# Kernel optimization log

Measured on AMD Instinct MI355X. Metric: run time of the kernel, lower is better.

## Reference

```python
import jax, jax.numpy as jnp
import numpy as np

E = 131072      # edges per key
MUL = 64        # multiplicity in '64x0e+64x1o'
FEA = MUL * 4   # 64 scalars + 64*3 vector components = 256
RAD = 64        # edge-length embedding width (64x0e)
HID = 128       # MLP hidden (128x0e)
WNUM = 4 * MUL  # 4 uvu paths x 64 per-channel weights = 256


def _mlp(x, W1, b1, g, be, W2):
    # Linear -> LayerNorm -> Gate(silu on scalars) -> last Linear (no bias)
    h = x @ W1 + b1
    mu = h.mean(-1, keepdims=True)
    var = h.var(-1, keepdims=True)
    h = (h - mu) / jnp.sqrt(var + 1e-5) * g + be
    return jax.nn.silu(h) @ W2


def _dtp(fea, vec, w):
    # depthwise (uvu) tensor product of (64x0e+64x1o) x (1x0e+1x1o) -> (64x0e+64x1o)
    x0 = fea[:, :MUL]                       # [E, 64]   0e part
    x1 = fea[:, MUL:].reshape(-1, MUL, 3)   # [E, 64, 3] 1o part
    y0 = vec[:, 0]                          # [E]       0e
    y1 = vec[:, 1:4]                        # [E, 3]    1o
    w1, w2, w3, w4 = jnp.split(w, 4, axis=1)  # each [E, 64]
    inv_s3 = 1.0 / jnp.sqrt(jnp.asarray(3.0, fea.dtype))  # CG(1,1,0) = delta/sqrt(3)
    inv_s2 = 1.0 / jnp.sqrt(jnp.asarray(2.0, fea.dtype))  # per-output path normalization (2 paths each)
    out0 = (w1 * x0 * y0[:, None]
            + w4 * jnp.einsum('eud,ed->eu', x1, y1) * inv_s3) * inv_s2
    out1 = (w2[:, :, None] * x0[:, :, None] * y1[:, None, :]
            + w3[:, :, None] * x1 * y0[:, None, None]) * inv_s2
    return jnp.concatenate([out0, out1.reshape(-1, MUL * 3)], axis=1)


def setup_inputs() -> dict:
    key = jax.random.key(0)
    ks = jax.random.split(key, 16)
    d = {}
    for i, k in enumerate(['a', 'b']):
        d[f'edge_fea_{k}'] = jax.random.normal(ks[i * 3 + 0], (E, FEA), jnp.float32)
        d[f'edge_vec_{k}'] = jax.random.normal(ks[i * 3 + 1], (E, 4), jnp.float32)
        d[f'edge_len_{k}'] = jax.random.uniform(ks[i * 3 + 2], (E, RAD), jnp.float32)
        d[f'W1_{k}'] = jax.random.normal(ks[6 + i * 2], (RAD, HID), jnp.float32) / np.sqrt(RAD)
        d[f'b1_{k}'] = jnp.zeros((HID,), jnp.float32)
        d[f'g_{k}'] = jnp.ones((HID,), jnp.float32)
        d[f'be_{k}'] = jnp.zeros((HID,), jnp.float32)
        d[f'W2_{k}'] = jax.random.normal(ks[10 + i * 2], (HID, WNUM), jnp.float32) / np.sqrt(HID)
    return d


def reference(edge_fea_a, edge_vec_a, edge_len_a, W1_a, b1_a, g_a, be_a, W2_a,
              edge_fea_b, edge_vec_b, edge_len_b, W1_b, b1_b, g_b, be_b, W2_b):
    wa = _mlp(edge_len_a, W1_a, b1_a, g_a, be_a, W2_a)
    wb = _mlp(edge_len_b, W1_b, b1_b, g_b, be_b, W2_b)
    return (_dtp(edge_fea_a, edge_vec_a, wa), _dtp(edge_fea_b, edge_vec_b, wb))
```

## Files before the change

kernel.cpp:

```cpp
#include <hip/hip_runtime.h>

namespace {
constexpr int E_N  = 131072;
constexpr int FEA  = 256;
constexpr int RAD  = 64;
constexpr int HID  = 128;
constexpr int WN   = 256;
constexpr int EPB  = 64;
constexpr int NT   = 256;
constexpr int LSTR = 68;
constexpr int ASTR = 132;
constexpr int SMEMF = EPB * ASTR;
constexpr int FRAG_HI_SHORTS = 2 * 4 * 16 * 64 * 8;
constexpr int W1HI = 2 * FRAG_HI_SHORTS;
constexpr int W1LO_DELTA = 2 * 2 * 8 * 64 * 8;
}

typedef short short8v __attribute__((ext_vector_type(8)));
typedef float floatx4 __attribute__((ext_vector_type(4)));

__device__ __forceinline__ unsigned bf16rne(float x) {
    const unsigned u = __float_as_uint(x);
    return (u + 0x7FFFu + ((u >> 16) & 1u)) >> 16;
}
__device__ __forceinline__ float bf16tof(unsigned h) {
    return __uint_as_float(h << 16);
}
__device__ __forceinline__ void bf16split(float x, unsigned& hi, unsigned& lo) {
    hi = bf16rne(x);
    lo = bf16rne(x - bf16tof(hi));
}

union FragU { uint4 u; short8v v; };

__global__ __launch_bounds__(64)
void prep_w2(const float* __restrict__ W2a, const float* __restrict__ W2b,
             unsigned short* __restrict__ frag)
{
    const int lane = threadIdx.x;
    const int nb = blockIdx.x, kt = blockIdx.y, pipe = blockIdx.z;
    const float* __restrict__ W2 = pipe ? W2b : W2a;
    const int g = lane >> 4, s = lane & 15;
    unsigned ph[4], pl[4];
    #pragma unroll
    for (int p = 0; p < 4; ++p) {
        const float x0 = W2[(size_t)(32*kt + 8*g + 2*p)     * WN + nb*16 + s];
        const float x1 = W2[(size_t)(32*kt + 8*g + 2*p + 1) * WN + nb*16 + s];
        unsigned h0, l0, h1, l1;
        bf16split(x0, h0, l0);
        bf16split(x1, h1, l1);
        ph[p] = h0 | (h1 << 16);
        pl[p] = l0 | (l1 << 16);
    }
    const size_t fi = (size_t)pipe * 32768 + (size_t)((kt*16 + nb)*64 + lane) * 8;
    *(uint4*)(frag + fi)                  = make_uint4(ph[0], ph[1], ph[2], ph[3]);
    *(uint4*)(frag + FRAG_HI_SHORTS + fi) = make_uint4(pl[0], pl[1], pl[2], pl[3]);
}

__global__ __launch_bounds__(64)
void prep_w1(const float* __restrict__ W1a, const float* __restrict__ W1b,
             unsigned short* __restrict__ frag)
{
    const int lane = threadIdx.x;
    const int nb = blockIdx.x, kt = blockIdx.y, pipe = blockIdx.z;
    const float* __restrict__ W1 = pipe ? W1b : W1a;
    const int g = lane >> 4, s = lane & 15;
    unsigned ph[4], pl[4];
    #pragma unroll
    for (int p = 0; p < 4; ++p) {
        const float x0 = W1[(size_t)(32*kt + 8*g + 2*p)     * HID + nb*16 + s];
        const float x1 = W1[(size_t)(32*kt + 8*g + 2*p + 1) * HID + nb*16 + s];
        unsigned h0, l0, h1, l1;
        bf16split(x0, h0, l0);
        bf16split(x1, h1, l1);
        ph[p] = h0 | (h1 << 16);
        pl[p] = l0 | (l1 << 16);
    }
    const size_t fi = (size_t)W1HI + (size_t)pipe * 8192
                    + (size_t)((kt*8 + nb)*64 + lane) * 8;
    *(uint4*)(frag + fi)              = make_uint4(ph[0], ph[1], ph[2], ph[3]);
    *(uint4*)(frag + W1LO_DELTA + fi) = make_uint4(pl[0], pl[1], pl[2], pl[3]);
}

__global__ __launch_bounds__(NT, 4)
void fused_mlp_dtp(
    const float* __restrict__ fea_a, const float* __restrict__ vec_a,
    const float* __restrict__ len_a, const float* __restrict__ b1_a,
    const float* __restrict__ g_a,   const float* __restrict__ be_a,
    const float* __restrict__ fea_b, const float* __restrict__ vec_b,
    const float* __restrict__ len_b, const float* __restrict__ b1_b,
    const float* __restrict__ g_b,   const float* __restrict__ be_b,
    const unsigned short* __restrict__ fragW,
    float* __restrict__ out)
{
    __shared__ __align__(16) float smem[SMEMF];

    const int pipe = blockIdx.y;
    const float* __restrict__ fea = pipe ? fea_b : fea_a;
    const float* __restrict__ vec = pipe ? vec_b : vec_a;
    const float* __restrict__ len = pipe ? len_b : len_a;
    const float* __restrict__ b1  = pipe ? b1_b  : b1_a;
    const float* __restrict__ g   = pipe ? g_b   : g_a;
    const float* __restrict__ be  = pipe ? be_b  : be_a;
    float* __restrict__ outp = out + (size_t)pipe * (size_t)E_N * FEA;

    const int t    = threadIdx.x;
    const int lane = t & 63;
    const int wv_  = t >> 6;
    const int s_   = lane & 15, g_ = lane >> 4;
    const long e0  = (long)blockIdx.x * EPB;

    {
        const float4* __restrict__ src = (const float4*)(len + e0 * RAD);
        #pragma unroll
        for (int i = 0; i < (EPB * RAD / 4) / NT; ++i) {
            const int f = t + i * NT;
            const float4 v = src[f];
            const int e = f >> 4, kq = (f & 15) * 4;
            *(float4*)(&smem[e * LSTR + kq]) = v;
        }
    }
    __syncthreads();

    floatx4 acc2[8];
    #pragma unroll
    for (int nb = 0; nb < 8; ++nb) {
        acc2[nb][0] = 0.f; acc2[nb][1] = 0.f; acc2[nb][2] = 0.f; acc2[nb][3] = 0.f;
    }
    {
        const int eA = wv_ * 16 + s_;
        const unsigned short* __restrict__ fH1 = fragW + W1HI + (size_t)pipe * 8192;
        const unsigned short* __restrict__ fL1 = fH1 + W1LO_DELTA;
        #pragma unroll
        for (int kt = 0; kt < 2; ++kt) {
            float xs[8];
            {
                const float4 x0 = *(const float4*)(&smem[eA*LSTR + 32*kt + 8*g_]);
                const float4 x1 = *(const float4*)(&smem[eA*LSTR + 32*kt + 8*g_ + 4]);
                xs[0]=x0.x; xs[1]=x0.y; xs[2]=x0.z; xs[3]=x0.w;
                xs[4]=x1.x; xs[5]=x1.y; xs[6]=x1.z; xs[7]=x1.w;
            }
            FragU ahu, alu;
            {
                unsigned ph[4], pl[4];
                #pragma unroll
                for (int p = 0; p < 4; ++p) {
                    unsigned h0, l0, h1, l1;
                    bf16split(xs[2*p],     h0, l0);
                    bf16split(xs[2*p + 1], h1, l1);
                    ph[p] = h0 | (h1 << 16);
                    pl[p] = l0 | (l1 << 16);
                }
                ahu.u = make_uint4(ph[0], ph[1], ph[2], ph[3]);
                alu.u = make_uint4(pl[0], pl[1], pl[2], pl[3]);
            }
            const short8v ah = ahu.v, al = alu.v;
            const size_t kb = (size_t)(kt * 8) * 512 + (size_t)lane * 8;
            #pragma unroll
            for (int nb = 0; nb < 8; ++nb) {
                const short8v bh = *(const short8v*)(fH1 + kb + nb * 512);
                const short8v bl = *(const short8v*)(fL1 + kb + nb * 512);
                acc2[nb] = __builtin_amdgcn_mfma_f32_16x16x32_bf16(ah, bh, acc2[nb], 0, 0, 0);
                acc2[nb] = __builtin_amdgcn_mfma_f32_16x16x32_bf16(ah, bl, acc2[nb], 0, 0, 0);
                acc2[nb] = __builtin_amdgcn_mfma_f32_16x16x32_bf16(al, bh, acc2[nb], 0, 0, 0);
            }
        }
    }
    __syncthreads();

    {
        float hv[8][4];
        float sum[4] = {0.f, 0.f, 0.f, 0.f};
        float sq [4] = {0.f, 0.f, 0.f, 0.f};
        #pragma unroll
        for (int nb = 0; nb < 8; ++nb) {
            const float b1v = b1[16*nb + s_];
            #pragma unroll
            for (int r = 0; r < 4; ++r) {
                const float v = acc2[nb][r] + b1v;
                hv[nb][r] = v;
                sum[r] += v;
                sq [r] += v * v;
            }
        }
        float mu[4], iv[4];
        #pragma unroll
        for (int r = 0; r < 4; ++r) {
            float s1 = sum[r], s2 = sq[r];
            s1 += __shfl_xor(s1, 1); s1 += __shfl_xor(s1, 2);
            s1 += __shfl_xor(s1, 4); s1 += __shfl_xor(s1, 8);
            s2 += __shfl_xor(s2, 1); s2 += __shfl_xor(s2, 2);
            s2 += __shfl_xor(s2, 4); s2 += __shfl_xor(s2, 8);
            mu[r] = s1 * (1.0f / HID);
            float var = s2 * (1.0f / HID) - mu[r] * mu[r];
            var = fmaxf(var, 0.0f);
            iv[r] = rsqrtf(var + 1e-5f);
        }
        const int rowb = wv_ * 16 + 4 * g_;
        #pragma unroll
        for (int nb = 0; nb < 8; ++nb) {
            const float gv  = g [16*nb + s_];
            const float bev = be[16*nb + s_];
            #pragma unroll
            for (int r = 0; r < 4; ++r) {
                const float hn = (hv[nb][r] - mu[r]) * iv[r] * gv + bev;
                const float sl = hn / (1.0f + __expf(-hn));
                smem[(rowb + r) * ASTR + 16*nb + s_] = sl;
            }
        }
    }
    __syncthreads();

    floatx4 acc[16];
    #pragma unroll
    for (int nb = 0; nb < 16; ++nb) {
        acc[nb][0] = 0.f; acc[nb][1] = 0.f; acc[nb][2] = 0.f; acc[nb][3] = 0.f;
    }
    {
        const int eA = wv_ * 16 + s_;
        const unsigned short* __restrict__ fH = fragW + (size_t)pipe * 32768;
        const unsigned short* __restrict__ fL = fH + FRAG_HI_SHORTS;
        for (int kt = 0; kt < 4; ++kt) {
            float xs[8];
            {
                const float4 x0 = *(const float4*)(&smem[eA*ASTR + 32*kt + 8*g_]);
                const float4 x1 = *(const float4*)(&smem[eA*ASTR + 32*kt + 8*g_ + 4]);
                xs[0]=x0.x; xs[1]=x0.y; xs[2]=x0.z; xs[3]=x0.w;
                xs[4]=x1.x; xs[5]=x1.y; xs[6]=x1.z; xs[7]=x1.w;
            }
            FragU ahu, alu;
            {
                unsigned ph[4], pl[4];
                #pragma unroll
                for (int p = 0; p < 4; ++p) {
                    unsigned h0, l0, h1, l1;
                    bf16split(xs[2*p],     h0, l0);
                    bf16split(xs[2*p + 1], h1, l1);
                    ph[p] = h0 | (h1 << 16);
                    pl[p] = l0 | (l1 << 16);
                }
                ahu.u = make_uint4(ph[0], ph[1], ph[2], ph[3]);
                alu.u = make_uint4(pl[0], pl[1], pl[2], pl[3]);
            }
            const short8v ah = ahu.v, al = alu.v;
            const size_t kb = (size_t)(kt * 16) * 512 + (size_t)lane * 8;
            #pragma unroll
            for (int nb = 0; nb < 16; ++nb) {
                const short8v bh = *(const short8v*)(fH + kb + nb * 512);
                const short8v bl = *(const short8v*)(fL + kb + nb * 512);
                acc[nb] = __builtin_amdgcn_mfma_f32_16x16x32_bf16(ah, bh, acc[nb], 0, 0, 0);
                acc[nb] = __builtin_amdgcn_mfma_f32_16x16x32_bf16(ah, bl, acc[nb], 0, 0, 0);
                acc[nb] = __builtin_amdgcn_mfma_f32_16x16x32_bf16(al, bh, acc[nb], 0, 0, 0);
            }
        }
    }
    __syncthreads();

    {
        const float c2 = 0.70710678118654752f;
        const float c3 = 0.40824829046386302f;
        float* sStage = smem + wv_ * 784;
        for (int r = 0; r < 4; ++r) {
            const long e = e0 + wv_ * 16 + 4 * g_ + r;
            const float4 y = *(const float4*)(vec + e * 4);
            const float* __restrict__ fr   = fea  + e * (size_t)FEA;
            float* __restrict__       orow = outp + e * (size_t)FEA;
            #pragma unroll
            for (int q = 0; q < 4; ++q) {
                const int u = 16 * q + s_;
                const float w1 = acc[q     ][r];
                const float w2 = acc[q + 4 ][r];
                const float w3 = acc[q + 8 ][r];
                const float w4 = acc[q + 12][r];
                const float x0  = fr[u];
                const float x1a = fr[64 + 3*u + 0];
                const float x1b = fr[64 + 3*u + 1];
                const float x1c = fr[64 + 3*u + 2];
                const float dot = x1a*y.y + x1b*y.z + x1c*y.w;
                orow[u] = w1*x0*y.x*c2 + w4*dot*c3;
                sStage[g_*196 + 3*u + 0] = (w2*x0*y.y + w3*x1a*y.x) * c2;
                sStage[g_*196 + 3*u + 1] = (w2*x0*y.z + w3*x1b*y.x) * c2;
                sStage[g_*196 + 3*u + 2] = (w2*x0*y.w + w3*x1c*y.x) * c2;
            }
            __syncthreads();
            #pragma unroll
            for (int rr = 0; rr < 3; ++rr) {
                const int flat = rr * 256 + lane * 4;
                const int eloc = flat / 192;
                const int pos  = flat % 192;
                const float4 v = *(const float4*)(&sStage[eloc * 196 + pos]);
                *(float4*)(&outp[(e0 + wv_*16 + 4*eloc + r) * (size_t)FEA + 64 + pos]) = v;
            }
            __syncthreads();
        }
    }
}

extern "C" void kernel_launch(void* const* d_in, const int* in_sizes, int n_in,
                              void* d_out, int out_size, void* d_ws, size_t ws_size,
                              hipStream_t stream) {
    (void)in_sizes; (void)n_in; (void)ws_size; (void)out_size;
    const float* fea_a = (const float*)d_in[0];
    const float* vec_a = (const float*)d_in[1];
    const float* len_a = (const float*)d_in[2];
    const float* W1_a  = (const float*)d_in[3];
    const float* b1_a  = (const float*)d_in[4];
    const float* g_a   = (const float*)d_in[5];
    const float* be_a  = (const float*)d_in[6];
    const float* W2_a  = (const float*)d_in[7];
    const float* fea_b = (const float*)d_in[8];
    const float* vec_b = (const float*)d_in[9];
    const float* len_b = (const float*)d_in[10];
    const float* W1_b  = (const float*)d_in[11];
    const float* b1_b  = (const float*)d_in[12];
    const float* g_b   = (const float*)d_in[13];
    const float* be_b  = (const float*)d_in[14];
    const float* W2_b  = (const float*)d_in[15];
    float* out = (float*)d_out;
    unsigned short* frag = (unsigned short*)d_ws;

    hipLaunchKernelGGL(prep_w2, dim3(16, 4, 2), dim3(64), 0, stream,
                       W2_a, W2_b, frag);
    hipLaunchKernelGGL(prep_w1, dim3(8, 2, 2), dim3(64), 0, stream,
                       W1_a, W1_b, frag);

    dim3 grid(E_N / EPB, 2);
    dim3 block(NT);
    hipLaunchKernelGGL(fused_mlp_dtp, grid, block, 0, stream,
                       fea_a, vec_a, len_a, b1_a, g_a, be_a,
                       fea_b, vec_b, len_b, b1_b, g_b, be_b,
                       frag, out);
}
```

Measured before the change: 180.9 us.

## Store activations as pre-split bf16 in swizzled LDS and drop block barriers

The LayerNorm/SiLU stage now writes hi/lo bf16 halves of each activation into XOR-swizzled LDS, so the second GEMM loads ready-made MFMA fragments instead of re-splitting floats per kt. Block-wide __syncthreads are replaced with wave-local lgkmcnt waits, on the basis that each wave reads only rows it wrote itself. LDS is reorganized to 32KB and launch bounds are raised to 5 blocks per SM to improve occupancy. The risk is the wave-local fence: the final staging region (wave*4096 bytes) overlaps activation rows that other waves may still be reading, which could race.

```diff
diff --git a/kernel.cpp b/kernel.cpp
--- a/kernel.cpp
+++ b/kernel.cpp
@@ -9,8 +9,6 @@
 constexpr int EPB  = 64;
 constexpr int NT   = 256;
 constexpr int LSTR = 68;
-constexpr int ASTR = 132;
-constexpr int SMEMF = EPB * ASTR;
 constexpr int FRAG_HI_SHORTS = 2 * 4 * 16 * 64 * 8;
 constexpr int W1HI = 2 * FRAG_HI_SHORTS;
 constexpr int W1LO_DELTA = 2 * 2 * 8 * 64 * 8;
@@ -30,6 +28,11 @@
     hi = bf16rne(x);
     lo = bf16rne(x - bf16tof(hi));
 }
+
+#define LDS_FENCE() do { \
+    asm volatile("s_waitcnt lgkmcnt(0)" ::: "memory"); \
+    __builtin_amdgcn_sched_barrier(0); \
+} while (0)
 
 union FragU { uint4 u; short8v v; };
 
@@ -82,7 +85,7 @@
     *(uint4*)(frag + W1LO_DELTA + fi) = make_uint4(pl[0], pl[1], pl[2], pl[3]);
 }
 
-__global__ __launch_bounds__(NT, 4)
+__global__ __launch_bounds__(NT, 5)
 void fused_mlp_dtp(
     const float* __restrict__ fea_a, const float* __restrict__ vec_a,
     const float* __restrict__ len_a, const float* __restrict__ b1_a,
@@ -93,7 +96,10 @@
     const unsigned short* __restrict__ fragW,
     float* __restrict__ out)
 {
-    __shared__ __align__(16) float smem[SMEMF];
+    __shared__ __align__(16) char smemraw[32768];
+    float*          lenT = (float*)smemraw;
+    unsigned short* actH = (unsigned short*)smemraw;
+    unsigned short* actL = (unsigned short*)(smemraw + 16384);
 
     const int pipe = blockIdx.y;
     const float* __restrict__ fea = pipe ? fea_b : fea_a;
@@ -117,7 +123,7 @@
             const int f = t + i * NT;
             const float4 v = src[f];
             const int e = f >> 4, kq = (f & 15) * 4;
-            *(float4*)(&smem[e * LSTR + kq]) = v;
+            *(float4*)(&lenT[e * LSTR + kq]) = v;
         }
     }
     __syncthreads();
@@ -135,8 +141,8 @@
         for (int kt = 0; kt < 2; ++kt) {
             float xs[8];
             {
-                const float4 x0 = *(const float4*)(&smem[eA*LSTR + 32*kt + 8*g_]);
-                const float4 x1 = *(const float4*)(&smem[eA*LSTR + 32*kt + 8*g_ + 4]);
+                const float4 x0 = *(const float4*)(&lenT[eA*LSTR + 32*kt + 8*g_]);
+                const float4 x1 = *(const float4*)(&lenT[eA*LSTR + 32*kt + 8*g_ + 4]);
                 xs[0]=x0.x; xs[1]=x0.y; xs[2]=x0.z; xs[3]=x0.w;
                 xs[4]=x1.x; xs[5]=x1.y; xs[6]=x1.z; xs[7]=x1.w;
             }
@@ -201,15 +207,21 @@
         for (int nb = 0; nb < 8; ++nb) {
             const float gv  = g [16*nb + s_];
             const float bev = be[16*nb + s_];
+            const int blkbase = 2*nb + (s_ >> 3);
             #pragma unroll
             for (int r = 0; r < 4; ++r) {
                 const float hn = (hv[nb][r] - mu[r]) * iv[r] * gv + bev;
                 const float sl = hn / (1.0f + __expf(-hn));
-                smem[(rowb + r) * ASTR + 16*nb + s_] = sl;
-            }
-        }
-    }
-    __syncthreads();
+                unsigned h, l;
+                bf16split(sl, h, l);
+                const int e = rowb + r;
+                const int idx = e * 128 + ((blkbase ^ (e & 7)) << 3) + (s_ & 7);
+                actH[idx] = (unsigned short)h;
+                actL[idx] = (unsigned short)l;
+            }
+        }
+    }
+    LDS_FENCE();
 
     floatx4 acc[16];
     #pragma unroll
@@ -221,27 +233,10 @@
         const unsigned short* __restrict__ fH = fragW + (size_t)pipe * 32768;
         const unsigned short* __restrict__ fL = fH + FRAG_HI_SHORTS;
         for (int kt = 0; kt < 4; ++kt) {
-            float xs[8];
-            {
-                const float4 x0 = *(const float4*)(&smem[eA*ASTR + 32*kt + 8*g_]);
-                const float4 x1 = *(const float4*)(&smem[eA*ASTR + 32*kt + 8*g_ + 4]);
-                xs[0]=x0.x; xs[1]=x0.y; xs[2]=x0.z; xs[3]=x0.w;
-                xs[4]=x1.x; xs[5]=x1.y; xs[6]=x1.z; xs[7]=x1.w;
-            }
+            const int sg = (4*kt + g_) ^ (s_ & 7);
             FragU ahu, alu;
-            {
-                unsigned ph[4], pl[4];
-                #pragma unroll
-                for (int p = 0; p < 4; ++p) {
-                    unsigned h0, l0, h1, l1;
-                    bf16split(xs[2*p],     h0, l0);
-                    bf16split(xs[2*p + 1], h1, l1);
-                    ph[p] = h0 | (h1 << 16);
-                    pl[p] = l0 | (l1 << 16);
-                }
-                ahu.u = make_uint4(ph[0], ph[1], ph[2], ph[3]);
-                alu.u = make_uint4(pl[0], pl[1], pl[2], pl[3]);
-            }
+            ahu.u = *(const uint4*)(actH + eA * 128 + sg * 8);
+            alu.u = *(const uint4*)(actL + eA * 128 + sg * 8);
             const short8v ah = ahu.v, al = alu.v;
             const size_t kb = (size_t)(kt * 16) * 512 + (size_t)lane * 8;
             #pragma unroll
@@ -254,12 +249,12 @@
             }
         }
     }
-    __syncthreads();
+    LDS_FENCE();
 
     {
         const float c2 = 0.70710678118654752f;
         const float c3 = 0.40824829046386302f;
-        float* sStage = smem + wv_ * 784;
+        float* sStage = (float*)(smemraw + wv_ * 4096);
         for (int r = 0; r < 4; ++r) {
             const long e = e0 + wv_ * 16 + 4 * g_ + r;
             const float4 y = *(const float4*)(vec + e * 4);
@@ -282,7 +277,7 @@
                 sStage[g_*196 + 3*u + 1] = (w2*x0*y.z + w3*x1b*y.x) * c2;
                 sStage[g_*196 + 3*u + 2] = (w2*x0*y.w + w3*x1c*y.x) * c2;
             }
-            __syncthreads();
+            LDS_FENCE();
             #pragma unroll
             for (int rr = 0; rr < 3; ++rr) {
                 const int flat = rr * 256 + lane * 4;
@@ -291,7 +286,7 @@
                 const float4 v = *(const float4*)(&sStage[eloc * 196 + pos]);
                 *(float4*)(&outp[(e0 + wv_*16 + 4*eloc + r) * (size_t)FEA + 64 + pos]) = v;
             }
-            __syncthreads();
+            LDS_FENCE();
         }
     }
 }
```

Result: slower. 298.2 us (+64.8%).

## Process two 16-row M-blocks per wave to reuse weight fragments

Applied to the files above, without the earlier changes.

Doubles edges per block from 64 to 128 so each wave computes two 16-edge MFMA row tiles, reusing every loaded W1/W2 bf16 fragment across both tiles. This halves weight-fragment global/L2 loads per edge and the number of blocks. In exchange accumulator register use roughly doubles, so launch bounds drop to 2 blocks per SM-equivalent, lowering occupancy for the memory-bound DTP epilogue. The shared-memory buffer is sized from EPB, so its size grows with the tile.

```diff
diff --git a/kernel.cpp b/kernel.cpp
--- a/kernel.cpp
+++ b/kernel.cpp
@@ -6,7 +6,7 @@
 constexpr int RAD  = 64;
 constexpr int HID  = 128;
 constexpr int WN   = 256;
-constexpr int EPB  = 64;
+constexpr int EPB  = 128;
 constexpr int NT   = 256;
 constexpr int LSTR = 68;
 constexpr int ASTR = 132;
@@ -82,7 +82,7 @@
     *(uint4*)(frag + W1LO_DELTA + fi) = make_uint4(pl[0], pl[1], pl[2], pl[3]);
 }
 
-__global__ __launch_bounds__(NT, 4)
+__global__ __launch_bounds__(NT, 2)
 void fused_mlp_dtp(
     const float* __restrict__ fea_a, const float* __restrict__ vec_a,
     const float* __restrict__ len_a, const float* __restrict__ b1_a,
@@ -108,6 +108,7 @@
     const int lane = t & 63;
     const int wv_  = t >> 6;
     const int s_   = lane & 15, g_ = lane >> 4;
+    const int ew   = wv_ * 32;
     const long e0  = (long)blockIdx.x * EPB;
 
     {
@@ -122,26 +123,29 @@
     }
     __syncthreads();
 
-    floatx4 acc2[8];
+    floatx4 acc2[2][8];
     #pragma unroll
-    for (int nb = 0; nb < 8; ++nb) {
-        acc2[nb][0] = 0.f; acc2[nb][1] = 0.f; acc2[nb][2] = 0.f; acc2[nb][3] = 0.f;
-    }
-    {
-        const int eA = wv_ * 16 + s_;
+    for (int mb = 0; mb < 2; ++mb)
+        #pragma unroll
+        for (int nb = 0; nb < 8; ++nb) {
+            acc2[mb][nb][0] = 0.f; acc2[mb][nb][1] = 0.f;
+            acc2[mb][nb][2] = 0.f; acc2[mb][nb][3] = 0.f;
+        }
+    {
         const unsigned short* __restrict__ fH1 = fragW + W1HI + (size_t)pipe * 8192;
         const unsigned short* __restrict__ fL1 = fH1 + W1LO_DELTA;
         #pragma unroll
         for (int kt = 0; kt < 2; ++kt) {
-            float xs[8];
-            {
+            short8v ah[2], al[2];
+            #pragma unroll
+            for (int mb = 0; mb < 2; ++mb) {
+                const int eA = ew + mb * 16 + s_;
+                float xs[8];
                 const float4 x0 = *(const float4*)(&smem[eA*LSTR + 32*kt + 8*g_]);
                 const float4 x1 = *(const float4*)(&smem[eA*LSTR + 32*kt + 8*g_ + 4]);
                 xs[0]=x0.x; xs[1]=x0.y; xs[2]=x0.z; xs[3]=x0.w;
                 xs[4]=x1.x; xs[5]=x1.y; xs[6]=x1.z; xs[7]=x1.w;
-            }
-            FragU ahu, alu;
-            {
+                FragU ahu, alu;
                 unsigned ph[4], pl[4];
                 #pragma unroll
                 for (int p = 0; p < 4; ++p) {
@@ -153,83 +157,99 @@
                 }
                 ahu.u = make_uint4(ph[0], ph[1], ph[2], ph[3]);
                 alu.u = make_uint4(pl[0], pl[1], pl[2], pl[3]);
-            }
-            const short8v ah = ahu.v, al = alu.v;
+                ah[mb] = ahu.v; al[mb] = alu.v;
+            }
             const size_t kb = (size_t)(kt * 8) * 512 + (size_t)lane * 8;
             #pragma unroll
             for (int nb = 0; nb < 8; ++nb) {
                 const short8v bh = *(const short8v*)(fH1 + kb + nb * 512);
                 const short8v bl = *(const short8v*)(fL1 + kb + nb * 512);
-                acc2[nb] = __builtin_amdgcn_mfma_f32_16x16x32_bf16(ah, bh, acc2[nb], 0, 0, 0);
-                acc2[nb] = __builtin_amdgcn_mfma_f32_16x16x32_bf16(ah, bl, acc2[nb], 0, 0, 0);
-                acc2[nb] = __builtin_amdgcn_mfma_f32_16x16x32_bf16(al, bh, acc2[nb], 0, 0, 0);
+                #pragma unroll
+                for (int mb = 0; mb < 2; ++mb) {
+                    acc2[mb][nb] = __builtin_amdgcn_mfma_f32_16x16x32_bf16(ah[mb], bh, acc2[mb][nb], 0, 0, 0);
+                    acc2[mb][nb] = __builtin_amdgcn_mfma_f32_16x16x32_bf16(ah[mb], bl, acc2[mb][nb], 0, 0, 0);
+                    acc2[mb][nb] = __builtin_amdgcn_mfma_f32_16x16x32_bf16(al[mb], bh, acc2[mb][nb], 0, 0, 0);
+                }
             }
         }
     }
     __syncthreads();
 
     {
-        float hv[8][4];
-        float sum[4] = {0.f, 0.f, 0.f, 0.f};
-        float sq [4] = {0.f, 0.f, 0.f, 0.f};
+        float hv[2][8][4];
+        float sum[2][4], sq[2][4];
+        #pragma unroll
+        for (int mb = 0; mb < 2; ++mb)
+            #pragma unroll
+            for (int r = 0; r < 4; ++r) { sum[mb][r] = 0.f; sq[mb][r] = 0.f; }
         #pragma unroll
         for (int nb = 0; nb < 8; ++nb) {
             const float b1v = b1[16*nb + s_];
             #pragma unroll
+            for (int mb = 0; mb < 2; ++mb)
+                #pragma unroll
+                for (int r = 0; r < 4; ++r) {
+                    const float v = acc2[mb][nb][r] + b1v;
+                    hv[mb][nb][r] = v;
+                    sum[mb][r] += v;
+                    sq [mb][r] += v * v;
+                }
+        }
+        float mu[2][4], iv[2][4];
+        #pragma unroll
+        for (int mb = 0; mb < 2; ++mb)
+            #pragma unroll
             for (int r = 0; r < 4; ++r) {
-                const float v = acc2[nb][r] + b1v;
-                hv[nb][r] = v;
-                sum[r] += v;
-                sq [r] += v * v;
-            }
-        }
-        float mu[4], iv[4];
-        #pragma unroll
-        for (int r = 0; r < 4; ++r) {
-            float s1 = sum[r], s2 = sq[r];
-            s1 += __shfl_xor(s1, 1); s1 += __shfl_xor(s1, 2);
-            s1 += __shfl_xor(s1, 4); s1 += __shfl_xor(s1, 8);
-            s2 += __shfl_xor(s2, 1); s2 += __shfl_xor(s2, 2);
-            s2 += __shfl_xor(s2, 4); s2 += __shfl_xor(s2, 8);
-            mu[r] = s1 * (1.0f / HID);
-            float var = s2 * (1.0f / HID) - mu[r] * mu[r];
-            var = fmaxf(var, 0.0f);
-            iv[r] = rsqrtf(var + 1e-5f);
-        }
-        const int rowb = wv_ * 16 + 4 * g_;
+                float s1 = sum[mb][r], s2 = sq[mb][r];
+                s1 += __shfl_xor(s1, 1); s1 += __shfl_xor(s1, 2);
+                s1 += __shfl_xor(s1, 4); s1 += __shfl_xor(s1, 8);
+                s2 += __shfl_xor(s2, 1); s2 += __shfl_xor(s2, 2);
+                s2 += __shfl_xor(s2, 4); s2 += __shfl_xor(s2, 8);
+                mu[mb][r] = s1 * (1.0f / HID);
+                float var = s2 * (1.0f / HID) - mu[mb][r] * mu[mb][r];
+                var = fmaxf(var, 0.0f);
+                iv[mb][r] = rsqrtf(var + 1e-5f);
+            }
         #pragma unroll
         for (int nb = 0; nb < 8; ++nb) {
             const float gv  = g [16*nb + s_];
             const float bev = be[16*nb + s_];
             #pragma unroll
-            for (int r = 0; r < 4; ++r) {
-                const float hn = (hv[nb][r] - mu[r]) * iv[r] * gv + bev;
-                const float sl = hn / (1.0f + __expf(-hn));
-                smem[(rowb + r) * ASTR + 16*nb + s_] = sl;
+            for (int mb = 0; mb < 2; ++mb) {
+                const int rowb = ew + 16*mb + 4*g_;
+                #pragma unroll
+                for (int r = 0; r < 4; ++r) {
+                    const float hn = (hv[mb][nb][r] - mu[mb][r]) * iv[mb][r] * gv + bev;
+                    const float sl = hn / (1.0f + __expf(-hn));
+                    smem[(rowb + r) * ASTR + 16*nb + s_] = sl;
+                }
             }
         }
     }
     __syncthreads();
 
-    floatx4 acc[16];
+    floatx4 acc[2][16];
     #pragma unroll
-    for (int nb = 0; nb < 16; ++nb) {
-        acc[nb][0] = 0.f; acc[nb][1] = 0.f; acc[nb][2] = 0.f; acc[nb][3] = 0.f;
-    }
-    {
-        const int eA = wv_ * 16 + s_;
+    for (int mb = 0; mb < 2; ++mb)
+        #pragma unroll
+        for (int nb = 0; nb < 16; ++nb) {
+            acc[mb][nb][0] = 0.f; acc[mb][nb][1] = 0.f;
+            acc[mb][nb][2] = 0.f; acc[mb][nb][3] = 0.f;
+        }
+    {
         const unsigned short* __restrict__ fH = fragW + (size_t)pipe * 32768;
         const unsigned short* __restrict__ fL = fH + FRAG_HI_SHORTS;
         for (int kt = 0; kt < 4; ++kt) {
-            float xs[8];
-            {
+            short8v ah[2], al[2];
+            #pragma unroll
+            for (int mb = 0; mb < 2; ++mb) {
+                const int eA = ew + mb * 16 + s_;
+                float xs[8];
                 const float4 x0 = *(const float4*)(&smem[eA*ASTR + 32*kt + 8*g_]);
                 const float4 x1 = *(const float4*)(&smem[eA*ASTR + 32*kt + 8*g_ + 4]);
                 xs[0]=x0.x; xs[1]=x0.y; xs[2]=x0.z; xs[3]=x0.w;
                 xs[4]=x1.x; xs[5]=x1.y; xs[6]=x1.z; xs[7]=x1.w;
-            }
-            FragU ahu, alu;
-            {
+                FragU ahu, alu;
                 unsigned ph[4], pl[4];
                 #pragma unroll
                 for (int p = 0; p < 4; ++p) {
@@ -241,16 +261,19 @@
                 }
                 ahu.u = make_uint4(ph[0], ph[1], ph[2], ph[3]);
                 alu.u = make_uint4(pl[0], pl[1], pl[2], pl[3]);
-            }
-            const short8v ah = ahu.v, al = alu.v;
+                ah[mb] = ahu.v; al[mb] = alu.v;
+            }
             const size_t kb = (size_t)(kt * 16) * 512 + (size_t)lane * 8;
             #pragma unroll
             for (int nb = 0; nb < 16; ++nb) {
                 const short8v bh = *(const short8v*)(fH + kb + nb * 512);
                 const short8v bl = *(const short8v*)(fL + kb + nb * 512);
-                acc[nb] = __builtin_amdgcn_mfma_f32_16x16x32_bf16(ah, bh, acc[nb], 0, 0, 0);
-                acc[nb] = __builtin_amdgcn_mfma_f32_16x16x32_bf16(ah, bl, acc[nb], 0, 0, 0);
-                acc[nb] = __builtin_amdgcn_mfma_f32_16x16x32_bf16(al, bh, acc[nb], 0, 0, 0);
+                #pragma unroll
+                for (int mb = 0; mb < 2; ++mb) {
+                    acc[mb][nb] = __builtin_amdgcn_mfma_f32_16x16x32_bf16(ah[mb], bh, acc[mb][nb], 0, 0, 0);
+                    acc[mb][nb] = __builtin_amdgcn_mfma_f32_16x16x32_bf16(ah[mb], bl, acc[mb][nb], 0, 0, 0);
+                    acc[mb][nb] = __builtin_amdgcn_mfma_f32_16x16x32_bf16(al[mb], bh, acc[mb][nb], 0, 0, 0);
+                }
             }
         }
     }
@@ -260,38 +283,41 @@
         const float c2 = 0.70710678118654752f;
         const float c3 = 0.40824829046386302f;
         float* sStage = smem + wv_ * 784;
-        for (int r = 0; r < 4; ++r) {
-            const long e = e0 + wv_ * 16 + 4 * g_ + r;
-            const float4 y = *(const float4*)(vec + e * 4);
-            const float* __restrict__ fr   = fea  + e * (size_t)FEA;
-            float* __restrict__       orow = outp + e * (size_t)FEA;
-            #pragma unroll
-            for (int q = 0; q < 4; ++q) {
-                const int u = 16 * q + s_;
-                const float w1 = acc[q     ][r];
-                const float w2 = acc[q + 4 ][r];
-                const float w3 = acc[q + 8 ][r];
-                const float w4 = acc[q + 12][r];
-                const float x0  = fr[u];
-                const float x1a = fr[64 + 3*u + 0];
-                const float x1b = fr[64 + 3*u + 1];
-                const float x1c = fr[64 + 3*u + 2];
-                const float dot = x1a*y.y + x1b*y.z + x1c*y.w;
-                orow[u] = w1*x0*y.x*c2 + w4*dot*c3;
-                sStage[g_*196 + 3*u + 0] = (w2*x0*y.y + w3*x1a*y.x) * c2;
-                sStage[g_*196 + 3*u + 1] = (w2*x0*y.z + w3*x1b*y.x) * c2;
-                sStage[g_*196 + 3*u + 2] = (w2*x0*y.w + w3*x1c*y.x) * c2;
-            }
-            __syncthreads();
-            #pragma unroll
-            for (int rr = 0; rr < 3; ++rr) {
-                const int flat = rr * 256 + lane * 4;
-                const int eloc = flat / 192;
-                const int pos  = flat % 192;
-                const float4 v = *(const float4*)(&sStage[eloc * 196 + pos]);
-                *(float4*)(&outp[(e0 + wv_*16 + 4*eloc + r) * (size_t)FEA + 64 + pos]) = v;
-            }
-            __syncthreads();
+        #pragma unroll
+        for (int mb = 0; mb < 2; ++mb) {
+            for (int r = 0; r < 4; ++r) {
+                const long e = e0 + ew + 16*mb + 4*g_ + r;
+                const float4 y = *(const float4*)(vec + e * 4);
+                const float* __restrict__ fr   = fea  + e * (size_t)FEA;
+                float* __restrict__       orow = outp + e * (size_t)FEA;
+                #pragma unroll
+                for (int q = 0; q < 4; ++q) {
+                    const int u = 16 * q + s_;
+                    const float w1 = acc[mb][q     ][r];
+                    const float w2 = acc[mb][q + 4 ][r];
+                    const float w3 = acc[mb][q + 8 ][r];
+                    const float w4 = acc[mb][q + 12][r];
+                    const float x0  = fr[u];
+                    const float x1a = fr[64 + 3*u + 0];
+                    const float x1b = fr[64 + 3*u + 1];
+                    const float x1c = fr[64 + 3*u + 2];
+                    const float dot = x1a*y.y + x1b*y.z + x1c*y.w;
+                    orow[u] = w1*x0*y.x*c2 + w4*dot*c3;
+                    sStage[g_*196 + 3*u + 0] = (w2*x0*y.y + w3*x1a*y.x) * c2;
+                    sStage[g_*196 + 3*u + 1] = (w2*x0*y.z + w3*x1b*y.x) * c2;
+                    sStage[g_*196 + 3*u + 2] = (w2*x0*y.w + w3*x1c*y.x) * c2;
+                }
+                __syncthreads();
+                #pragma unroll
+                for (int rr = 0; rr < 3; ++rr) {
+                    const int flat = rr * 256 + lane * 4;
+                    const int eloc = flat / 192;
+                    const int pos  = flat % 192;
+                    const float4 v = *(const float4*)(&sStage[eloc * 196 + pos]);
+                    *(float4*)(&outp[(e0 + ew + 16*mb + 4*eloc + r) * (size_t)FEA + 64 + pos]) = v;
+                }
+                __syncthreads();
+            }
         }
     }
 }
```

Result: slower. 200.1 us (+10.6%).

## Read edge_len directly from global and batch two rows per staging barrier

Applied to the files above, without the earlier changes.

The first MLP layer now loads its edge_len fragments straight from global memory instead of staging them in shared memory, which removes one load pass and two block barriers. The output epilogue stages two edge-row groups per iteration in a larger per-wave shared buffer, halving the number of __syncthreads in the store loop. The cost is uncoalesced, strided per-lane global reads for the MLP input and more shared memory per wave (4 waves × 1568 floats still fits in SMEMF).

```diff
diff --git a/kernel.cpp b/kernel.cpp
--- a/kernel.cpp
+++ b/kernel.cpp
@@ -8,7 +8,6 @@
 constexpr int WN   = 256;
 constexpr int EPB  = 64;
 constexpr int NT   = 256;
-constexpr int LSTR = 68;
 constexpr int ASTR = 132;
 constexpr int SMEMF = EPB * ASTR;
 constexpr int FRAG_HI_SHORTS = 2 * 4 * 16 * 64 * 8;
@@ -110,33 +109,21 @@
     const int s_   = lane & 15, g_ = lane >> 4;
     const long e0  = (long)blockIdx.x * EPB;
 
-    {
-        const float4* __restrict__ src = (const float4*)(len + e0 * RAD);
-        #pragma unroll
-        for (int i = 0; i < (EPB * RAD / 4) / NT; ++i) {
-            const int f = t + i * NT;
-            const float4 v = src[f];
-            const int e = f >> 4, kq = (f & 15) * 4;
-            *(float4*)(&smem[e * LSTR + kq]) = v;
-        }
-    }
-    __syncthreads();
-
     floatx4 acc2[8];
     #pragma unroll
     for (int nb = 0; nb < 8; ++nb) {
         acc2[nb][0] = 0.f; acc2[nb][1] = 0.f; acc2[nb][2] = 0.f; acc2[nb][3] = 0.f;
     }
     {
-        const int eA = wv_ * 16 + s_;
+        const float* __restrict__ lrow = len + (e0 + wv_ * 16 + s_) * (size_t)RAD;
         const unsigned short* __restrict__ fH1 = fragW + W1HI + (size_t)pipe * 8192;
         const unsigned short* __restrict__ fL1 = fH1 + W1LO_DELTA;
         #pragma unroll
         for (int kt = 0; kt < 2; ++kt) {
             float xs[8];
             {
-                const float4 x0 = *(const float4*)(&smem[eA*LSTR + 32*kt + 8*g_]);
-                const float4 x1 = *(const float4*)(&smem[eA*LSTR + 32*kt + 8*g_ + 4]);
+                const float4 x0 = *(const float4*)(lrow + 32*kt + 8*g_);
+                const float4 x1 = *(const float4*)(lrow + 32*kt + 8*g_ + 4);
                 xs[0]=x0.x; xs[1]=x0.y; xs[2]=x0.z; xs[3]=x0.w;
                 xs[4]=x1.x; xs[5]=x1.y; xs[6]=x1.z; xs[7]=x1.w;
             }
@@ -166,7 +153,6 @@
             }
         }
     }
-    __syncthreads();
 
     {
         float hv[8][4];
@@ -259,38 +245,44 @@
     {
         const float c2 = 0.70710678118654752f;
         const float c3 = 0.40824829046386302f;
-        float* sStage = smem + wv_ * 784;
-        for (int r = 0; r < 4; ++r) {
-            const long e = e0 + wv_ * 16 + 4 * g_ + r;
-            const float4 y = *(const float4*)(vec + e * 4);
-            const float* __restrict__ fr   = fea  + e * (size_t)FEA;
-            float* __restrict__       orow = outp + e * (size_t)FEA;
-            #pragma unroll
-            for (int q = 0; q < 4; ++q) {
-                const int u = 16 * q + s_;
-                const float w1 = acc[q     ][r];
-                const float w2 = acc[q + 4 ][r];
-                const float w3 = acc[q + 8 ][r];
-                const float w4 = acc[q + 12][r];
-                const float x0  = fr[u];
-                const float x1a = fr[64 + 3*u + 0];
-                const float x1b = fr[64 + 3*u + 1];
-                const float x1c = fr[64 + 3*u + 2];
-                const float dot = x1a*y.y + x1b*y.z + x1c*y.w;
-                orow[u] = w1*x0*y.x*c2 + w4*dot*c3;
-                sStage[g_*196 + 3*u + 0] = (w2*x0*y.y + w3*x1a*y.x) * c2;
-                sStage[g_*196 + 3*u + 1] = (w2*x0*y.z + w3*x1b*y.x) * c2;
-                sStage[g_*196 + 3*u + 2] = (w2*x0*y.w + w3*x1c*y.x) * c2;
+        float* sStage = smem + wv_ * 1568;
+        for (int rp = 0; rp < 2; ++rp) {
+            #pragma unroll
+            for (int rr = 0; rr < 2; ++rr) {
+                const int r = rp * 2 + rr;
+                const long e = e0 + wv_ * 16 + 4 * g_ + r;
+                const float4 y = *(const float4*)(vec + e * 4);
+                const float* __restrict__ fr   = fea  + e * (size_t)FEA;
+                float* __restrict__       orow = outp + e * (size_t)FEA;
+                #pragma unroll
+                for (int q = 0; q < 4; ++q) {
+                    const int u = 16 * q + s_;
+                    const float w1 = acc[q     ][r];
+                    const float w2 = acc[q + 4 ][r];
+                    const float w3 = acc[q + 8 ][r];
+                    const float w4 = acc[q + 12][r];
+                    const float x0  = fr[u];
+                    const float x1a = fr[64 + 3*u + 0];
+                    const float x1b = fr[64 + 3*u + 1];
+                    const float x1c = fr[64 + 3*u + 2];
+                    const float dot = x1a*y.y + x1b*y.z + x1c*y.w;
+                    orow[u] = w1*x0*y.x*c2 + w4*dot*c3;
+                    sStage[rr*784 + g_*196 + 3*u + 0] = (w2*x0*y.y + w3*x1a*y.x) * c2;
+                    sStage[rr*784 + g_*196 + 3*u + 1] = (w2*x0*y.z + w3*x1b*y.x) * c2;
+                    sStage[rr*784 + g_*196 + 3*u + 2] = (w2*x0*y.w + w3*x1c*y.x) * c2;
+                }
             }
             __syncthreads();
             #pragma unroll
-            for (int rr = 0; rr < 3; ++rr) {
-                const int flat = rr * 256 + lane * 4;
-                const int eloc = flat / 192;
-                const int pos  = flat % 192;
-                const float4 v = *(const float4*)(&sStage[eloc * 196 + pos]);
-                *(float4*)(&outp[(e0 + wv_*16 + 4*eloc + r) * (size_t)FEA + 64 + pos]) = v;
-            }
+            for (int rr = 0; rr < 2; ++rr)
+                #pragma unroll
+                for (int dd = 0; dd < 3; ++dd) {
+                    const int flat = dd * 256 + lane * 4;
+                    const int eloc = flat / 192;
+                    const int pos  = flat % 192;
+                    const float4 v = *(const float4*)(&sStage[rr*784 + eloc*196 + pos]);
+                    *(float4*)(&outp[(e0 + wv_*16 + 4*eloc + rp*2 + rr) * (size_t)FEA + 64 + pos]) = v;
+                }
             __syncthreads();
         }
     }
```

Result: slower. 191.6 us (+5.9%).
